# Performance work log

Hardware: AMD Instinct MI355X
Metric: run time of the kernel (lower is better)

Reference implementation:

```python
import jax, jax.numpy as jnp
import numpy as np

EPS = 1e-5

def _layer_norm(x, gamma, beta):
    # LayerNorm over the last two dims [C, 128], matching nn.LayerNorm([C, 128])
    mean = jnp.mean(x, axis=(-2, -1), keepdims=True)
    var = jnp.var(x, axis=(-2, -1), keepdims=True)
    return (x - mean) * jax.lax.rsqrt(var + EPS) * gamma + beta


def setup_inputs() -> dict:
    key = jax.random.key(0)
    ks = jax.random.split(key, 7)
    B, C, N, L = 64, 1024, 128, 512
    W_SCALE = 0.02  # keep pre-softmax logits / activations in a sane range
    return {
        "X_in": jax.random.normal(ks[0], (B, C, N), jnp.float32),
        "T": jax.random.normal(ks[1], (B, C, L), jnp.float32),
        "Wq": jax.random.normal(ks[2], (C, C), jnp.float32) * W_SCALE,
        "Wk": jax.random.normal(ks[3], (C, C), jnp.float32) * W_SCALE,
        "Wv": jax.random.normal(ks[4], (C, C), jnp.float32) * W_SCALE,
        "Wf1": jax.random.normal(ks[5], (C, C), jnp.float32) * W_SCALE,
        "Wf2": jax.random.normal(ks[6], (C, C), jnp.float32) * W_SCALE,
        "gamma": jnp.ones((C, N), jnp.float32),
        "beta": jnp.zeros((C, N), jnp.float32),
    }


def reference(X_in, T, Wq, Wk, Wv, Wf1, Wf2, gamma, beta):
    C = Wq.shape[1]  # feature_map_cs (intended value of the buggy X_in.weight.shape[1])
    # 1x1 Conv1d == per-position channel matmul: weight [out, in]
    q = jnp.einsum('oc,bcn->bon', Wq, X_in)      # [B, C, N]
    k = jnp.einsum('oc,bcl->bol', Wk, T)         # [B, C, L]
    sim = jnp.einsum('bcn,bcl->bnl', q, k) / jnp.sqrt(jnp.float32(C))  # [B, N, L]
    attn = jax.nn.softmax(sim, axis=2)           # softmax over tokens L
    v = jnp.einsum('oc,bcl->bol', Wv, T)         # [B, C, L]
    ctx = jnp.einsum('bcl,bnl->bcn', v, attn)    # [B, C, N] == bmm(values, attn^T)
    X_out = _layer_norm(X_in + ctx, gamma, beta)
    h = jax.nn.relu(jnp.einsum('oc,bcn->bon', Wf1, X_out))
    ffn = jnp.einsum('oc,bcn->bon', Wf2, h)
    return _layer_norm(X_out + ffn, gamma, beta)
```

## Files before the change

### kernel.cpp

```cpp
#include <hip/hip_runtime.h>


using bf16   = __bf16;
using bf16x4 = __attribute__((ext_vector_type(4))) __bf16;
using bf16x8 = __attribute__((ext_vector_type(8))) __bf16;
using f32x4  = __attribute__((ext_vector_type(4))) float;

static constexpr int  Bb = 64;
static constexpr int  Cc = 1024;
static constexpr int  Nn = 128;
static constexpr int  Ll = 512;
static constexpr long long PLANE = (long long)Cc * Nn;
static constexpr float INV_PLANE = 1.0f / 131072.0f;

__device__ __forceinline__ void gload_lds16(const void* g, void* l) {
    __builtin_amdgcn_global_load_lds(
        (__attribute__((address_space(1))) void*)g,
        (__attribute__((address_space(3))) void*)l,
        16, 0, 0);
}

__global__ void __launch_bounds__(256)
prep_all(const float* __restrict__ Wv, const float* __restrict__ Wf1,
         const float* __restrict__ Wf2, const float* __restrict__ Wq,
         const float* __restrict__ Wk, const float* __restrict__ X,
         bf16* __restrict__ WvB, bf16* __restrict__ Wf1B, bf16* __restrict__ Wf2B,
         bf16* __restrict__ WqT, bf16* __restrict__ WkT, bf16* __restrict__ Xt) {
    __shared__ float tile[64][65];
    const int bx = blockIdx.x;
    const int t  = threadIdx.x;
    if (bx < 3072) {
        const float* in = bx < 1024 ? Wv : (bx < 2048 ? Wf1 : Wf2);
        bf16* out       = bx < 1024 ? WvB : (bx < 2048 ? Wf1B : Wf2B);
        int i = (bx & 1023) * 256 + t;
        float4 v = reinterpret_cast<const float4*>(in)[i];
        bf16x4 o = { (bf16)v.x, (bf16)v.y, (bf16)v.z, (bf16)v.w };
        reinterpret_cast<bf16x4*>(out)[i] = o;
        return;
    }
    const float* in; bf16* outT;
    int R, S, bxx, byy, bz = 0;
    if (bx < 3584) {
        int j = bx - 3072;
        in = (j >= 256) ? Wk : Wq; outT = (j >= 256) ? WkT : WqT;
        R = Cc; S = Cc; j &= 255; bxx = j & 15; byy = j >> 4;
    } else {
        int j = bx - 3584; bz = j >> 5; j &= 31;
        bxx = j & 1; byy = j >> 1; in = X; outT = Xt; R = Cc; S = Nn;
    }
    long long plane = (long long)R * S;
    in   += (long long)bz * plane;
    outT += (long long)bz * plane;
    int s0 = bxx * 64, r0 = byy * 64;
    int rl = t >> 4, sc = (t & 15) * 4;
    #pragma unroll
    for (int p = 0; p < 4; ++p) {
        int r = p * 16 + rl;
        float4 v = *(const float4*)(in + (long long)(r0 + r) * S + s0 + sc);
        *(float4*)&tile[r][sc] = v;
    }
    __syncthreads();
    long long tb = ((long long)(s0 >> 6) * (R >> 6) + (r0 >> 6)) * 4096;
    int sb = t >> 3, rg = (t & 7) * 8;
    #pragma unroll
    for (int p = 0; p < 2; ++p) {
        int s = sb + p * 32;
        bf16x8 o;
        #pragma unroll
        for (int j = 0; j < 8; ++j) o[j] = (bf16)tile[rg + j][s];
        *(bf16x8*)(outT + tb + s * 64 + rg) = o;
    }
}

#define GEMM_PROLOGUE_AND_LOOP(A_, Bt_, KLOOP_, LD_, TA_, TB_)                     \
    __shared__ bf16 As[2][128 * 64];                                               \
    __shared__ bf16 Bs[2][128 * 64];                                               \
    const int n0   = blockIdx.x * 128;                                             \
    const int m0   = blockIdx.y * 128;                                             \
    const int t    = threadIdx.x;                                                  \
    const int lane = t & 63;                                                       \
    const int w    = t >> 6;                                                       \
    const int wr   = (w >> 1) * 64;                                                \
    const int wc   = (w & 1) * 64;                                                 \
    const int lr   = lane & 15;                                                    \
    const int hi4  = (lane >> 4) * 16;                                             \
    const int sw   = (lr & 7) << 4;                                                \
    const int stepA_ = (TA_) ? 4096 : 64;                                          \
    const int stepB_ = (TB_) ? 4096 : 64;                                          \
    const bf16* gA[4]; const bf16* gB[4]; int lo[4];                               \
    _Pragma("unroll")                                                              \
    for (int p = 0; p < 4; ++p) {                                                  \
        int o = w * 1024 + lane * 16 + p * 4096;                                   \
        int row = o >> 7;                                                          \
        int scol = ((o & 127) ^ ((row & 7) << 4)) >> 1;                            \
        lo[p] = o;                                                                 \
        int ra = m0 + row, rb = n0 + row;                                          \
        gA[p] = (TA_) ? A_ + ((long long)(ra >> 6) * (LD_ >> 6)) * 4096            \
                           + (ra & 63) * 64 + scol                                 \
                      : A_ + (long long)ra * LD_ + scol;                           \
        gB[p] = (TB_) ? Bt_ + ((long long)(rb >> 6) * (LD_ >> 6)) * 4096           \
                            + (rb & 63) * 64 + scol                                \
                      : Bt_ + (long long)rb * LD_ + scol;                          \
    }                                                                              \
    f32x4 acc[4][4] = {};                                                          \
    const int NT_ = KLOOP_ / 64;                                                   \
    _Pragma("unroll")                                                              \
    for (int p = 0; p < 4; ++p) gload_lds16(gA[p], (char*)As[0] + lo[p]);          \
    _Pragma("unroll")                                                              \
    for (int p = 0; p < 4; ++p) gload_lds16(gB[p], (char*)Bs[0] + lo[p]);          \
    __syncthreads();                                                               \
    int cur_ = 0;                                                                  \
    for (int kt = 0; kt < NT_; ++kt) {                                             \
        if (kt + 1 < NT_) {                                                        \
            _Pragma("unroll")                                                      \
            for (int p = 0; p < 4; ++p)                                            \
                gload_lds16(gA[p] + (long long)(kt + 1) * stepA_,                  \
                            (char*)As[cur_ ^ 1] + lo[p]);                          \
            _Pragma("unroll")                                                      \
            for (int p = 0; p < 4; ++p)                                            \
                gload_lds16(gB[p] + (long long)(kt + 1) * stepB_,                  \
                            (char*)Bs[cur_ ^ 1] + lo[p]);                          \
        }                                                                          \
        const bf16* As_ = As[cur_]; const bf16* Bs_ = Bs[cur_];                    \
        _Pragma("unroll")                                                          \
        for (int kk = 0; kk < 2; ++kk) {                                           \
            bf16x8 af[4], bfr[4];                                                  \
            _Pragma("unroll")                                                      \
            for (int i = 0; i < 4; ++i) {                                          \
                int ra = wr + i * 16 + lr;                                         \
                int rb = wc + i * 16 + lr;                                         \
                af[i]  = *(const bf16x8*)((const char*)As_ +                       \
                          ((((ra << 7) + (kk << 6) + hi4)) ^ sw));                 \
                bfr[i] = *(const bf16x8*)((const char*)Bs_ +                       \
                          ((((rb << 7) + (kk << 6) + hi4)) ^ sw));                 \
            }                                                                      \
            _Pragma("unroll")                                                      \
            for (int mi = 0; mi < 4; ++mi)                                         \
                _Pragma("unroll")                                                  \
                for (int ni = 0; ni < 4; ++ni)                                     \
                    acc[mi][ni] = __builtin_amdgcn_mfma_f32_16x16x32_bf16(         \
                        af[mi], bfr[ni], acc[mi][ni], 0, 0, 0);                    \
        }                                                                          \
        __syncthreads();                                                           \
        cur_ ^= 1;                                                                 \
    }

template <typename OutT, bool RELU, int TA, int TB>
__global__ void __launch_bounds__(256, 2)
gemm_tn(const bf16* __restrict__ A, const bf16* __restrict__ Bt, OutT* __restrict__ C,
        int M, int N, int KLOOP, int ld, long long sA, long long sBt, long long sC,
        float scale) {
    A  += (long long)blockIdx.z * sA;
    Bt += (long long)blockIdx.z * sBt;
    C  += (long long)blockIdx.z * sC;
    GEMM_PROLOGUE_AND_LOOP(A, Bt, KLOOP, ld, TA, TB)
    const int rbase = m0 + wr + (lane >> 4) * 4;
    const int cbase = n0 + wc + lr;
    #pragma unroll
    for (int mi = 0; mi < 4; ++mi)
        #pragma unroll
        for (int ni = 0; ni < 4; ++ni)
            #pragma unroll
            for (int r = 0; r < 4; ++r) {
                float v = acc[mi][ni][r] * scale;
                if (RELU) v = fmaxf(v, 0.0f);
                C[(long long)(rbase + mi * 16 + r) * N + (cbase + ni * 16)] = (OutT)v;
            }
}

__global__ void g2_reduce(const float* __restrict__ p, bf16* __restrict__ g2) {
    int i = (blockIdx.x * 256 + threadIdx.x) * 4;
    float4 a = *(const float4*)(p + i);
    float4 b = *(const float4*)(p + 1048576 + i);
    float4 c = *(const float4*)(p + 2097152 + i);
    float4 d = *(const float4*)(p + 3145728 + i);
    bf16x4 o = { (bf16)(a.x + b.x + c.x + d.x), (bf16)(a.y + b.y + c.y + d.y),
                 (bf16)(a.z + b.z + c.z + d.z), (bf16)(a.w + b.w + c.w + d.w) };
    *(bf16x4*)(g2 + i) = o;
}

__global__ void __launch_bounds__(256, 2)
gemm_sim_exp(const bf16* __restrict__ A , const float* __restrict__ Tg,
             bf16* __restrict__ E, float* __restrict__ rspart) {
    __shared__ char smem[33024];
    bf16* Asb = (bf16*)smem;
    bf16* Bs  = (bf16*)(smem + 16384);
    bf16* scr = (bf16*)(smem + 24576);
    A  += (long long)blockIdx.z * ((long long)Nn * Cc);
    Tg += (long long)blockIdx.z * ((long long)Cc * Ll);
    E  += (long long)blockIdx.z * ((long long)Nn * Ll);
    const int l0 = blockIdx.x * 64;
    const int t = threadIdx.x, lane = t & 63, w = t >> 6;
    const int lr = lane & 15, hi4 = (lane >> 4) * 16, sw = (lr & 7) << 4;
    const bf16* gA[4]; int lo[4];
    #pragma unroll
    for (int p = 0; p < 4; ++p) {
        int o = w * 1024 + lane * 16 + p * 4096;
        int row = o >> 7;
        int scol = ((o & 127) ^ ((row & 7) << 4)) >> 1;
        lo[p] = o;
        gA[p] = A + (long long)row * Cc + scol;
    }
    const int s_c = t >> 2, s_l = (t & 3) * 16;
    float4 treg[4];
    #pragma unroll
    for (int i = 0; i < 4; ++i)
        treg[i] = *(const float4*)(Tg + (long long)s_c * Ll + l0 + s_l + i * 4);
    f32x4 acc[2][4] = {};
    const int NT = Cc / 64;
    for (int kt = 0; kt < NT; ++kt) {
        #pragma unroll
        for (int i = 0; i < 4; ++i) {
            float4 v = treg[i];
            bf16x4 o = { (bf16)v.x, (bf16)v.y, (bf16)v.z, (bf16)v.w };
            *(bf16x4*)(scr + s_c * 66 + s_l + i * 4) = o;
        }
        __syncthreads();
        #pragma unroll
        for (int p = 0; p < 4; ++p) gload_lds16(gA[p] + kt * 64, (char*)Asb + lo[p]);
        {
            int lrow = t & 63;
            #pragma unroll
            for (int p = 0; p < 2; ++p) {
                int c8 = (t >> 6) * 16 + p * 8;
                bf16x8 bv;
                #pragma unroll
                for (int j = 0; j < 8; ++j) bv[j] = scr[(c8 + j) * 66 + lrow];
                *(bf16x8*)((char*)Bs + (((lrow << 7) + c8 * 2) ^ ((lrow & 7) << 4))) = bv;
            }
        }
        if (kt + 1 < NT) {
            #pragma unroll
            for (int i = 0; i < 4; ++i)
                treg[i] = *(const float4*)(Tg + (long long)((kt + 1) * 64 + s_c) * Ll
                                           + l0 + s_l + i * 4);
        }
        __syncthreads();
        #pragma unroll
        for (int kk = 0; kk < 2; ++kk) {
            bf16x8 af[2], bfr[4];
            #pragma unroll
            for (int mi = 0; mi < 2; ++mi) {
                int ra = w * 32 + mi * 16 + lr;
                af[mi] = *(const bf16x8*)((const char*)Asb + (((ra << 7) + (kk << 6) + hi4) ^ sw));
            }
            #pragma unroll
            for (int ni = 0; ni < 4; ++ni) {
                int rb = ni * 16 + lr;
                bfr[ni] = *(const bf16x8*)((const char*)Bs + (((rb << 7) + (kk << 6) + hi4) ^ sw));
            }
            #pragma unroll
            for (int mi = 0; mi < 2; ++mi)
                #pragma unroll
                for (int ni = 0; ni < 4; ++ni)
                    acc[mi][ni] = __builtin_amdgcn_mfma_f32_16x16x32_bf16(
                        af[mi], bfr[ni], acc[mi][ni], 0, 0, 0);
        }
    }
    float psum[2][4];
    #pragma unroll
    for (int mi = 0; mi < 2; ++mi)
        #pragma unroll
        for (int r = 0; r < 4; ++r) psum[mi][r] = 0.f;
    #pragma unroll
    for (int mi = 0; mi < 2; ++mi)
        #pragma unroll
        for (int ni = 0; ni < 4; ++ni)
            #pragma unroll
            for (int r = 0; r < 4; ++r) {
                int row = w * 32 + mi * 16 + (lane >> 4) * 4 + r;
                float ev = __expf(acc[mi][ni][r] * 0.03125f);
                E[(long long)row * Ll + l0 + ni * 16 + lr] = (bf16)ev;
                psum[mi][r] += ev;
            }
    #pragma unroll
    for (int mi = 0; mi < 2; ++mi)
        #pragma unroll
        for (int r = 0; r < 4; ++r) {
            float v = psum[mi][r];
            v += __shfl_xor(v, 1); v += __shfl_xor(v, 2);
            v += __shfl_xor(v, 4); v += __shfl_xor(v, 8);
            psum[mi][r] = v;
        }
    if (lr == 0) {
        float* rp = rspart + ((long long)blockIdx.z * 8 + blockIdx.x) * 128;
        #pragma unroll
        for (int mi = 0; mi < 2; ++mi)
            #pragma unroll
            for (int r = 0; r < 4; ++r)
                rp[w * 32 + mi * 16 + (lane >> 4) * 4 + r] = psum[mi][r];
    }
}

__global__ void __launch_bounds__(256, 4)
gemm_u_scaled(const bf16* __restrict__ A , const float* __restrict__ Tg,
              bf16* __restrict__ C, const float* __restrict__ rspart) {
    __shared__ char smem[40960];
    bf16* AsB = (bf16*)smem;
    bf16* Bs  = (bf16*)(smem + 32768);
    A  += (long long)blockIdx.z * ((long long)Nn * Ll);
    Tg += (long long)blockIdx.z * ((long long)Cc * Ll);
    C  += (long long)blockIdx.z * ((long long)Nn * Cc);
    const float* rp = rspart + (long long)blockIdx.z * 1024;
    const int c0 = blockIdx.x * 64;
    const int t = threadIdx.x, lane = t & 63, w = t >> 6;
    const int lr = lane & 15, hi4 = (lane >> 4) * 16, sw = (lr & 7) << 4;
    const bf16* gA[4]; int lo[4];
    #pragma unroll
    for (int p = 0; p < 4; ++p) {
        int o = w * 1024 + lane * 16 + p * 4096;
        int row = o >> 7;
        int scol = ((o & 127) ^ ((row & 7) << 4)) >> 1;
        lo[p] = o;
        gA[p] = A + (long long)row * Ll + scol;
    }
    const int s_c = t >> 2, s_l = (t & 3) * 16;
    float4 treg[4];
    #pragma unroll
    for (int p = 0; p < 4; ++p) gload_lds16(gA[p], (char*)AsB + lo[p]);
    #pragma unroll
    for (int i = 0; i < 4; ++i)
        treg[i] = *(const float4*)(Tg + (long long)(c0 + s_c) * Ll + s_l + i * 4);
    f32x4 acc[2][4] = {};
    int cur = 0;
    const int NT = Ll / 64;
    for (int kt = 0; kt < NT; ++kt) {
        if (kt + 1 < NT) {
            #pragma unroll
            for (int p = 0; p < 4; ++p)
                gload_lds16(gA[p] + (kt + 1) * 64, (char*)AsB + (cur ^ 1) * 16384 + lo[p]);
        }
        __syncthreads();
        #pragma unroll
        for (int p = 0; p < 2; ++p) {
            bf16x8 bv;
            #pragma unroll
            for (int j = 0; j < 4; ++j) {
                bv[j]     = (bf16)((const float*)&treg[p * 2])[j];
                bv[4 + j] = (bf16)((const float*)&treg[p * 2 + 1])[j];
            }
            *(bf16x8*)((char*)Bs + (((s_c << 7) + (s_l + p * 8) * 2) ^ ((s_c & 7) << 4))) = bv;
        }
        if (kt + 1 < NT) {
            #pragma unroll
            for (int i = 0; i < 4; ++i)
                treg[i] = *(const float4*)(Tg + (long long)(c0 + s_c) * Ll
                                           + (kt + 1) * 64 + s_l + i * 4);
        }
        __syncthreads();
        const bf16* As_ = AsB + cur * 8192;
        #pragma unroll
        for (int kk = 0; kk < 2; ++kk) {
            bf16x8 af[2], bfr[4];
            #pragma unroll
            for (int mi = 0; mi < 2; ++mi) {
                int ra = w * 32 + mi * 16 + lr;
                af[mi] = *(const bf16x8*)((const char*)As_ + (((ra << 7) + (kk << 6) + hi4) ^ sw));
            }
            #pragma unroll
            for (int ni = 0; ni < 4; ++ni) {
                int rb = ni * 16 + lr;
                bfr[ni] = *(const bf16x8*)((const char*)Bs + (((rb << 7) + (kk << 6) + hi4) ^ sw));
            }
            #pragma unroll
            for (int mi = 0; mi < 2; ++mi)
                #pragma unroll
                for (int ni = 0; ni < 4; ++ni)
                    acc[mi][ni] = __builtin_amdgcn_mfma_f32_16x16x32_bf16(
                        af[mi], bfr[ni], acc[mi][ni], 0, 0, 0);
        }
        cur ^= 1;
    }
    #pragma unroll
    for (int mi = 0; mi < 2; ++mi)
        #pragma unroll
        for (int r = 0; r < 4; ++r) {
            int row = w * 32 + mi * 16 + (lane >> 4) * 4 + r;
            float s = 0.f;
            #pragma unroll
            for (int j = 0; j < 8; ++j) s += rp[j * 128 + row];
            float inv = 1.f / s;
            #pragma unroll
            for (int ni = 0; ni < 4; ++ni)
                C[(long long)row * Cc + (c0 + ni * 16 + lr)] = (bf16)(acc[mi][ni][r] * inv);
        }
}

__global__ void __launch_bounds__(256, 2)
gemm_ctx_ln1(const bf16* __restrict__ A , const bf16* __restrict__ Bt ,
             const float* __restrict__ X, bf16* __restrict__ Z1, float* __restrict__ partials,
             int K, long long sBt) {
    const int N = Nn;
    Bt += (long long)blockIdx.z * sBt;
    X  += (long long)blockIdx.z * PLANE;
    Z1 += (long long)blockIdx.z * PLANE;
    GEMM_PROLOGUE_AND_LOOP(A, Bt, K, K, 0, 0)
    const int rbase = m0 + wr + (lane >> 4) * 4;
    const int cbase = n0 + wc + lr;
    float s = 0.f, ss = 0.f;
    #pragma unroll
    for (int mi = 0; mi < 4; ++mi)
        #pragma unroll
        for (int ni = 0; ni < 4; ++ni)
            #pragma unroll
            for (int r = 0; r < 4; ++r) {
                long long idx = (long long)(rbase + mi * 16 + r) * N + (cbase + ni * 16);
                float zv = acc[mi][ni][r] + X[idx];
                Z1[idx] = (bf16)zv;
                s += zv; ss += zv * zv;
            }
    #pragma unroll
    for (int off = 32; off; off >>= 1) { s += __shfl_xor(s, off); ss += __shfl_xor(ss, off); }
    __shared__ float red[8];
    if (lane == 0) { red[w] = s; red[4 + w] = ss; }
    __syncthreads();
    if (t == 0) {
        float S = red[0] + red[1] + red[2] + red[3];
        float SS = red[4] + red[5] + red[6] + red[7];
        float* p = partials + ((long long)blockIdx.z * 8 + blockIdx.y) * 2;
        p[0] = S; p[1] = SS;
    }
}

__global__ void __launch_bounds__(256, 2)
gemm_ffn_ln2(const bf16* __restrict__ A , const bf16* __restrict__ Bt ,
             const bf16* __restrict__ Z1, const float* __restrict__ pp1,
             const float* __restrict__ gamma, const float* __restrict__ beta,
             bf16* __restrict__ Z2, float* __restrict__ partials,
             int K, long long sA) {
    A  += (long long)blockIdx.z * sA;
    Z1 += (long long)blockIdx.z * PLANE;
    Z2 += (long long)blockIdx.z * PLANE;
    float S1 = 0.f, SS1 = 0.f;
    #pragma unroll
    for (int j = 0; j < 8; ++j) {
        S1  += pp1[((long long)blockIdx.z * 8 + j) * 2];
        SS1 += pp1[((long long)blockIdx.z * 8 + j) * 2 + 1];
    }
    const float mean1 = S1 * INV_PLANE;
    const float rstd1 = rsqrtf(SS1 * INV_PLANE - mean1 * mean1 + 1e-5f);
    GEMM_PROLOGUE_AND_LOOP(A, Bt, K, K, 0, 0)
    const int rbase = m0 + wr + (lane >> 4) * 4;
    const int cbase = n0 + wc + lr;
    float s = 0.f, ss = 0.f;
    #pragma unroll
    for (int mi = 0; mi < 4; ++mi)
        #pragma unroll
        for (int ni = 0; ni < 4; ++ni) {
            long long a = (long long)(cbase + ni * 16) * Nn + rbase + mi * 16;
            bf16x4 z1v = *(const bf16x4*)(Z1 + a);
            float4 g  = *(const float4*)(gamma + a);
            float4 be = *(const float4*)(beta + a);
            float x0 = ((float)z1v[0] - mean1) * rstd1 * g.x + be.x;
            float x1 = ((float)z1v[1] - mean1) * rstd1 * g.y + be.y;
            float x2 = ((float)z1v[2] - mean1) * rstd1 * g.z + be.z;
            float x3 = ((float)z1v[3] - mean1) * rstd1 * g.w + be.w;
            float z0 = acc[mi][ni][0] + x0, z1 = acc[mi][ni][1] + x1;
            float z2 = acc[mi][ni][2] + x2, z3 = acc[mi][ni][3] + x3;
            bf16x4 zo = { (bf16)z0, (bf16)z1, (bf16)z2, (bf16)z3 };
            *(bf16x4*)(Z2 + a) = zo;
            s  += z0 + z1 + z2 + z3;
            ss += z0 * z0 + z1 * z1 + z2 * z2 + z3 * z3;
        }
    #pragma unroll
    for (int off = 32; off; off >>= 1) { s += __shfl_xor(s, off); ss += __shfl_xor(ss, off); }
    __shared__ float red[8];
    if (lane == 0) { red[w] = s; red[4 + w] = ss; }
    __syncthreads();
    if (t == 0) {
        float S = red[0] + red[1] + red[2] + red[3];
        float SS = red[4] + red[5] + red[6] + red[7];
        float* p = partials + ((long long)blockIdx.z * 8 + blockIdx.x) * 2;
        p[0] = S; p[1] = SS;
    }
}

__global__ void ln1_norm_transpose(const bf16* __restrict__ Z1, const float* __restrict__ partials,
                                   const float* __restrict__ gamma, const float* __restrict__ beta,
                                   bf16* __restrict__ XoutT) {
    int b = blockIdx.z;
    float S = 0.f, SS = 0.f;
    #pragma unroll
    for (int j = 0; j < 8; ++j) {
        S  += partials[((long long)b * 8 + j) * 2];
        SS += partials[((long long)b * 8 + j) * 2 + 1];
    }
    float mean = S * INV_PLANE;
    float rstd = rsqrtf(SS * INV_PLANE - mean * mean + 1e-5f);
    __shared__ float tile[64][65];
    long long base = (long long)b * PLANE;
    int n0 = blockIdx.x * 64, c0 = blockIdx.y * 64;
    int t = threadIdx.x;
    int rl = t >> 4, sc = (t & 15) * 4;
    #pragma unroll
    for (int p = 0; p < 4; ++p) {
        int r = p * 16 + rl;
        long long idx = (long long)(c0 + r) * Nn + n0 + sc;
        bf16x4 z  = *(const bf16x4*)(Z1 + base + idx);
        float4 g  = *(const float4*)(gamma + idx);
        float4 be = *(const float4*)(beta + idx);
        float4 o = {((float)z[0] - mean) * rstd * g.x + be.x,
                    ((float)z[1] - mean) * rstd * g.y + be.y,
                    ((float)z[2] - mean) * rstd * g.z + be.z,
                    ((float)z[3] - mean) * rstd * g.w + be.w};
        *(float4*)&tile[r][sc] = o;
    }
    __syncthreads();
    long long tb = ((long long)(n0 >> 6) * (Cc >> 6) + (c0 >> 6)) * 4096;
    int sb = t >> 3, rg = (t & 7) * 8;
    #pragma unroll
    for (int p = 0; p < 2; ++p) {
        int n = sb + p * 32;
        bf16x8 o;
        #pragma unroll
        for (int j = 0; j < 8; ++j) o[j] = (bf16)tile[rg + j][n];
        *(bf16x8*)(XoutT + base + tb + n * 64 + rg) = o;
    }
}

__global__ void ln2_final(const bf16* __restrict__ Z2, const float* __restrict__ partials,
                          const float* __restrict__ gamma, const float* __restrict__ beta,
                          float* __restrict__ out) {
    int b = blockIdx.y;
    float S = 0.f, SS = 0.f;
    #pragma unroll
    for (int j = 0; j < 8; ++j) {
        S  += partials[((long long)b * 8 + j) * 2];
        SS += partials[((long long)b * 8 + j) * 2 + 1];
    }
    float mean = S * INV_PLANE;
    float rstd = rsqrtf(SS * INV_PLANE - mean * mean + 1e-5f);
    long long base = (long long)b * PLANE;
    int i = (blockIdx.x * 256 + threadIdx.x) * 8;
    bf16x8 z = *(const bf16x8*)(Z2 + base + i);
    #pragma unroll
    for (int h = 0; h < 2; ++h) {
        float4 g  = *(const float4*)(gamma + i + h * 4);
        float4 be = *(const float4*)(beta + i + h * 4);
        float4 o = {((float)z[h * 4 + 0] - mean) * rstd * g.x + be.x,
                    ((float)z[h * 4 + 1] - mean) * rstd * g.y + be.y,
                    ((float)z[h * 4 + 2] - mean) * rstd * g.z + be.z,
                    ((float)z[h * 4 + 3] - mean) * rstd * g.w + be.w};
        *(float4*)(out + base + i + h * 4) = o;
    }
}

extern "C" void kernel_launch(void* const* d_in, const int* in_sizes, int n_in,
                              void* d_out, int out_size, void* d_ws, size_t ws_size,
                              hipStream_t stream) {
    const float* X   = (const float*)d_in[0];
    const float* T   = (const float*)d_in[1];
    const float* Wq  = (const float*)d_in[2];
    const float* Wk  = (const float*)d_in[3];
    const float* Wv  = (const float*)d_in[4];
    const float* Wf1 = (const float*)d_in[5];
    const float* Wf2 = (const float*)d_in[6];
    const float* gamma = (const float*)d_in[7];
    const float* beta  = (const float*)d_in[8];
    float* out = (float*)d_out;
    char* ws = (char*)d_ws;
    const size_t MB = 1ull << 20;

    bf16* WvB  = (bf16*)(ws + 0 * MB);
    bf16* Wf1B = (bf16*)(ws + 2 * MB);
    bf16* Wf2B = (bf16*)(ws + 4 * MB);
    bf16* WqT  = (bf16*)(ws + 6 * MB);
    bf16* WkT  = (bf16*)(ws + 8 * MB);
    bf16* G2   = (bf16*)(ws + 10 * MB);
    bf16* Xt   = (bf16*)(ws + 12 * MB);
    bf16* Z1   = (bf16*)(ws + 28 * MB);
    bf16* XoutT= (bf16*)(ws + 44 * MB);
    bf16* hT   = (bf16*)(ws + 60 * MB);
    bf16* e    = (bf16*)(ws + 76 * MB);
    bf16* Z2   = (bf16*)(ws + 92 * MB);
    bf16* E    = (bf16*)(ws + 108 * MB);
    bf16* u    = (bf16*)(ws + 116 * MB);
    float* G2p = (float*)(ws + 132 * MB);
    float* pp1 = (float*)(ws + 148 * MB);
    float* pp2 = (float*)(ws + 148 * MB + 65536);
    float* rsp = (float*)(ws + 149 * MB);

    dim3 blk256(256);

    prep_all<<<dim3(5632), blk256, 0, stream>>>(
        Wv, Wf1, Wf2, Wq, Wk, X, WvB, Wf1B, Wf2B, WqT, WkT, Xt);

    gemm_tn<float, false, 1, 1><<<dim3(8, 8, 4), blk256, 0, stream>>>(
        WkT, WqT, G2p, Cc, Cc, 256, Cc, 16384, 16384, 1048576, 1.f);
    g2_reduce<<<dim3(1024), blk256, 0, stream>>>(G2p, G2);

    gemm_tn<bf16, false, 1, 0><<<dim3(8, 1, Bb), blk256, 0, stream>>>(
        Xt, G2, e, Nn, Cc, Cc, Cc, (long long)Nn * Cc, 0, (long long)Nn * Cc, 1.f);
    gemm_sim_exp<<<dim3(8, 1, Bb), blk256, 0, stream>>>(e, T, E, rsp);
    gemm_u_scaled<<<dim3(16, 1, Bb), blk256, 0, stream>>>(E, T, u, rsp);
    gemm_ctx_ln1<<<dim3(1, 8, Bb), blk256, 0, stream>>>(
        WvB, u, X, Z1, pp1, Cc, (long long)Nn * Cc);
    ln1_norm_transpose<<<dim3(Nn / 64, Cc / 64, Bb), blk256, 0, stream>>>(
        Z1, pp1, gamma, beta, XoutT);
    gemm_tn<bf16, true, 1, 0><<<dim3(8, 1, Bb), blk256, 0, stream>>>(
        XoutT, Wf1B, hT, Nn, Cc, Cc, Cc, (long long)Nn * Cc, 0, (long long)Nn * Cc, 1.f);
    gemm_ffn_ln2<<<dim3(8, 1, Bb), blk256, 0, stream>>>(
        hT, Wf2B, Z1, pp1, gamma, beta, Z2, pp2, Cc, (long long)Nn * Cc);
    ln2_final<<<dim3(64, Bb), blk256, 0, stream>>>(Z2, pp2, gamma, beta, out);
}
```

Baseline: 258.0 us.

## Fuse fp32-to-bf16 conversion of weights and X into GEMM operand loads

Drops the upfront conversion and transpose of Wv, Wf1, Wf2 and X to bf16. Four GEMM kernels now load fp32 operands straight from global memory into registers, convert them to bf16 and write them swizzled into LDS. For X this includes an in-LDS transpose through a scratch buffer, with the next tile prefetched into registers. This removes a prep pass and its global round-trip. In exchange, every batch block re-reads and re-converts the fp32 weights, doubling operand bytes and adding conversion ALU work inside the main loops, which are now single-buffered for that operand.

```diff
diff --git a/kernel.cpp b/kernel.cpp
--- a/kernel.cpp
+++ b/kernel.cpp
@@ -21,53 +21,32 @@
 }
 
 __global__ void __launch_bounds__(256)
-prep_all(const float* __restrict__ Wv, const float* __restrict__ Wf1,
-         const float* __restrict__ Wf2, const float* __restrict__ Wq,
-         const float* __restrict__ Wk, const float* __restrict__ X,
-         bf16* __restrict__ WvB, bf16* __restrict__ Wf1B, bf16* __restrict__ Wf2B,
-         bf16* __restrict__ WqT, bf16* __restrict__ WkT, bf16* __restrict__ Xt) {
+prep_w(const float* __restrict__ Wq, const float* __restrict__ Wk,
+       bf16* __restrict__ WqT, bf16* __restrict__ WkT) {
     __shared__ float tile[64][65];
-    const int bx = blockIdx.x;
-    const int t  = threadIdx.x;
-    if (bx < 3072) {
-        const float* in = bx < 1024 ? Wv : (bx < 2048 ? Wf1 : Wf2);
-        bf16* out       = bx < 1024 ? WvB : (bx < 2048 ? Wf1B : Wf2B);
-        int i = (bx & 1023) * 256 + t;
-        float4 v = reinterpret_cast<const float4*>(in)[i];
-        bf16x4 o = { (bf16)v.x, (bf16)v.y, (bf16)v.z, (bf16)v.w };
-        reinterpret_cast<bf16x4*>(out)[i] = o;
-        return;
-    }
-    const float* in; bf16* outT;
-    int R, S, bxx, byy, bz = 0;
-    if (bx < 3584) {
-        int j = bx - 3072;
-        in = (j >= 256) ? Wk : Wq; outT = (j >= 256) ? WkT : WqT;
-        R = Cc; S = Cc; j &= 255; bxx = j & 15; byy = j >> 4;
-    } else {
-        int j = bx - 3584; bz = j >> 5; j &= 31;
-        bxx = j & 1; byy = j >> 1; in = X; outT = Xt; R = Cc; S = Nn;
-    }
-    long long plane = (long long)R * S;
-    in   += (long long)bz * plane;
-    outT += (long long)bz * plane;
+    int j = blockIdx.x;
+    const float* in = (j >= 256) ? Wk : Wq;
+    bf16* outT      = (j >= 256) ? WkT : WqT;
+    j &= 255;
+    int bxx = j & 15, byy = j >> 4;
     int s0 = bxx * 64, r0 = byy * 64;
+    int t = threadIdx.x;
     int rl = t >> 4, sc = (t & 15) * 4;
     #pragma unroll
     for (int p = 0; p < 4; ++p) {
         int r = p * 16 + rl;
-        float4 v = *(const float4*)(in + (long long)(r0 + r) * S + s0 + sc);
+        float4 v = *(const float4*)(in + (long long)(r0 + r) * Cc + s0 + sc);
         *(float4*)&tile[r][sc] = v;
     }
     __syncthreads();
-    long long tb = ((long long)(s0 >> 6) * (R >> 6) + (r0 >> 6)) * 4096;
+    long long tb = ((long long)(s0 >> 6) * (Cc >> 6) + (r0 >> 6)) * 4096;
     int sb = t >> 3, rg = (t & 7) * 8;
     #pragma unroll
     for (int p = 0; p < 2; ++p) {
         int s = sb + p * 32;
         bf16x8 o;
         #pragma unroll
-        for (int j = 0; j < 8; ++j) o[j] = (bf16)tile[rg + j][s];
+        for (int jj = 0; jj < 8; ++jj) o[jj] = (bf16)tile[rg + jj][s];
         *(bf16x8*)(outT + tb + s * 64 + rg) = o;
     }
 }
@@ -180,6 +159,92 @@
 }
 
 __global__ void __launch_bounds__(256, 2)
+gemm_e(const float* __restrict__ Xg, const bf16* __restrict__ G2, bf16* __restrict__ e) {
+    __shared__ char smem[49664];
+    bf16* Asl = (bf16*)smem;
+    bf16* Bs  = (bf16*)(smem + 16384);
+    bf16* scr = (bf16*)(smem + 32768);
+    Xg += (long long)blockIdx.z * PLANE;
+    e  += (long long)blockIdx.z * ((long long)Nn * Cc);
+    const int n0 = blockIdx.x * 128;
+    const int t = threadIdx.x, lane = t & 63, w = t >> 6;
+    const int wr = (w >> 1) * 64, wc = (w & 1) * 64;
+    const int lr = lane & 15, hi4 = (lane >> 4) * 16, sw = (lr & 7) << 4;
+    const bf16* gB[4]; int lo[4];
+    #pragma unroll
+    for (int p = 0; p < 4; ++p) {
+        int o = w * 1024 + lane * 16 + p * 4096;
+        int row = o >> 7;
+        int scol = ((o & 127) ^ ((row & 7) << 4)) >> 1;
+        lo[p] = o;
+        gB[p] = G2 + (long long)(n0 + row) * Cc + scol;
+    }
+    const int s_c = t >> 2, s_n = (t & 3) * 32;
+    float4 xreg[8];
+    #pragma unroll
+    for (int i = 0; i < 8; ++i)
+        xreg[i] = *(const float4*)(Xg + (long long)s_c * Nn + s_n + i * 4);
+    f32x4 acc[4][4] = {};
+    const int NT = Cc / 64;
+    for (int kt = 0; kt < NT; ++kt) {
+        #pragma unroll
+        for (int i = 0; i < 8; ++i) {
+            float4 v = xreg[i];
+            bf16x4 o = { (bf16)v.x, (bf16)v.y, (bf16)v.z, (bf16)v.w };
+            *(bf16x4*)(scr + s_c * 130 + s_n + i * 4) = o;
+        }
+        __syncthreads();
+        #pragma unroll
+        for (int p = 0; p < 4; ++p) gload_lds16(gB[p] + kt * 64, (char*)Bs + lo[p]);
+        {
+            int nrow = t & 127;
+            #pragma unroll
+            for (int g = 0; g < 4; ++g) {
+                int c0 = (t >> 7) * 32 + g * 8;
+                bf16x8 bv;
+                #pragma unroll
+                for (int j = 0; j < 8; ++j) bv[j] = scr[(c0 + j) * 130 + nrow];
+                *(bf16x8*)((char*)Asl + (((nrow << 7) + c0 * 2) ^ ((nrow & 7) << 4))) = bv;
+            }
+        }
+        if (kt + 1 < NT) {
+            #pragma unroll
+            for (int i = 0; i < 8; ++i)
+                xreg[i] = *(const float4*)(Xg + (long long)((kt + 1) * 64 + s_c) * Nn
+                                           + s_n + i * 4);
+        }
+        __syncthreads();
+        #pragma unroll
+        for (int kk = 0; kk < 2; ++kk) {
+            bf16x8 af[4], bfr[4];
+            #pragma unroll
+            for (int i = 0; i < 4; ++i) {
+                int ra = wr + i * 16 + lr;
+                int rb = wc + i * 16 + lr;
+                af[i]  = *(const bf16x8*)((const char*)Asl + (((ra << 7) + (kk << 6) + hi4) ^ sw));
+                bfr[i] = *(const bf16x8*)((const char*)Bs  + (((rb << 7) + (kk << 6) + hi4) ^ sw));
+            }
+            #pragma unroll
+            for (int mi = 0; mi < 4; ++mi)
+                #pragma unroll
+                for (int ni = 0; ni < 4; ++ni)
+                    acc[mi][ni] = __builtin_amdgcn_mfma_f32_16x16x32_bf16(
+                        af[mi], bfr[ni], acc[mi][ni], 0, 0, 0);
+        }
+    }
+    const int rbase = wr + (lane >> 4) * 4;
+    const int cbase = n0 + wc + lr;
+    #pragma unroll
+    for (int mi = 0; mi < 4; ++mi)
+        #pragma unroll
+        for (int ni = 0; ni < 4; ++ni)
+            #pragma unroll
+            for (int r = 0; r < 4; ++r)
+                e[(long long)(rbase + mi * 16 + r) * Cc + (cbase + ni * 16)] =
+                    (bf16)acc[mi][ni][r];
+}
+
+__global__ void __launch_bounds__(256, 2)
 gemm_sim_exp(const bf16* __restrict__ A , const float* __restrict__ Tg,
              bf16* __restrict__ E, float* __restrict__ rspart) {
     __shared__ char smem[33024];
@@ -387,16 +452,76 @@
 }
 
 __global__ void __launch_bounds__(256, 2)
-gemm_ctx_ln1(const bf16* __restrict__ A , const bf16* __restrict__ Bt ,
-             const float* __restrict__ X, bf16* __restrict__ Z1, float* __restrict__ partials,
-             int K, long long sBt) {
-    const int N = Nn;
-    Bt += (long long)blockIdx.z * sBt;
+gemm_ctx_ln1(const float* __restrict__ Wv, const bf16* __restrict__ U,
+             const float* __restrict__ X, bf16* __restrict__ Z1, float* __restrict__ partials) {
+    __shared__ char smem[32768];
+    bf16* Asl = (bf16*)smem;
+    bf16* Bs  = (bf16*)(smem + 16384);
+    U  += (long long)blockIdx.z * ((long long)Nn * Cc);
     X  += (long long)blockIdx.z * PLANE;
     Z1 += (long long)blockIdx.z * PLANE;
-    GEMM_PROLOGUE_AND_LOOP(A, Bt, K, K, 0, 0)
+    const int m0 = blockIdx.y * 128;
+    const int t = threadIdx.x, lane = t & 63, w = t >> 6;
+    const int wr = (w >> 1) * 64, wc = (w & 1) * 64;
+    const int lr = lane & 15, hi4 = (lane >> 4) * 16, sw = (lr & 7) << 4;
+    const bf16* gB[4]; int lo[4];
+    #pragma unroll
+    for (int p = 0; p < 4; ++p) {
+        int o = w * 1024 + lane * 16 + p * 4096;
+        int row = o >> 7;
+        int scol = ((o & 127) ^ ((row & 7) << 4)) >> 1;
+        lo[p] = o;
+        gB[p] = U + (long long)row * Cc + scol;
+    }
+    const int s_r = t >> 1, s_k = (t & 1) * 32;
+    float4 wreg[8];
+    #pragma unroll
+    for (int i = 0; i < 8; ++i)
+        wreg[i] = *(const float4*)(Wv + (long long)(m0 + s_r) * Cc + s_k + i * 4);
+    f32x4 acc[4][4] = {};
+    const int NT = Cc / 64;
+    for (int kt = 0; kt < NT; ++kt) {
+        __syncthreads();
+        #pragma unroll
+        for (int p = 0; p < 4; ++p) gload_lds16(gB[p] + kt * 64, (char*)Bs + lo[p]);
+        #pragma unroll
+        for (int p = 0; p < 4; ++p) {
+            int kc = s_k + p * 8;
+            bf16x8 bv;
+            #pragma unroll
+            for (int j = 0; j < 4; ++j) {
+                bv[j]     = (bf16)((const float*)&wreg[p * 2])[j];
+                bv[4 + j] = (bf16)((const float*)&wreg[p * 2 + 1])[j];
+            }
+            *(bf16x8*)((char*)Asl + (((s_r << 7) + kc * 2) ^ ((s_r & 7) << 4))) = bv;
+        }
+        if (kt + 1 < NT) {
+            #pragma unroll
+            for (int i = 0; i < 8; ++i)
+                wreg[i] = *(const float4*)(Wv + (long long)(m0 + s_r) * Cc
+                                           + (kt + 1) * 64 + s_k + i * 4);
+        }
+        __syncthreads();
+        #pragma unroll
+        for (int kk = 0; kk < 2; ++kk) {
+            bf16x8 af[4], bfr[4];
+            #pragma unroll
+            for (int i = 0; i < 4; ++i) {
+                int ra = wr + i * 16 + lr;
+                int rb = wc + i * 16 + lr;
+                af[i]  = *(const bf16x8*)((const char*)Asl + (((ra << 7) + (kk << 6) + hi4) ^ sw));
+                bfr[i] = *(const bf16x8*)((const char*)Bs  + (((rb << 7) + (kk << 6) + hi4) ^ sw));
+            }
+            #pragma unroll
+            for (int mi = 0; mi < 4; ++mi)
+                #pragma unroll
+                for (int ni = 0; ni < 4; ++ni)
+                    acc[mi][ni] = __builtin_amdgcn_mfma_f32_16x16x32_bf16(
+                        af[mi], bfr[ni], acc[mi][ni], 0, 0, 0);
+        }
+    }
     const int rbase = m0 + wr + (lane >> 4) * 4;
-    const int cbase = n0 + wc + lr;
+    const int cbase = wc + lr;
     float s = 0.f, ss = 0.f;
     #pragma unroll
     for (int mi = 0; mi < 4; ++mi)
@@ -404,7 +529,7 @@
         for (int ni = 0; ni < 4; ++ni)
             #pragma unroll
             for (int r = 0; r < 4; ++r) {
-                long long idx = (long long)(rbase + mi * 16 + r) * N + (cbase + ni * 16);
+                long long idx = (long long)(rbase + mi * 16 + r) * Nn + (cbase + ni * 16);
                 float zv = acc[mi][ni][r] + X[idx];
                 Z1[idx] = (bf16)zv;
                 s += zv; ss += zv * zv;
@@ -423,12 +548,94 @@
 }
 
 __global__ void __launch_bounds__(256, 2)
-gemm_ffn_ln2(const bf16* __restrict__ A , const bf16* __restrict__ Bt ,
+gemm_h(const bf16* __restrict__ XoutT, const float* __restrict__ Wf1, bf16* __restrict__ hT) {
+    __shared__ char smem[32768];
+    bf16* Asl = (bf16*)smem;
+    bf16* Bs  = (bf16*)(smem + 16384);
+    XoutT += (long long)blockIdx.z * PLANE;
+    hT    += (long long)blockIdx.z * ((long long)Nn * Cc);
+    const int n0 = blockIdx.x * 128;
+    const int t = threadIdx.x, lane = t & 63, w = t >> 6;
+    const int wr = (w >> 1) * 64, wc = (w & 1) * 64;
+    const int lr = lane & 15, hi4 = (lane >> 4) * 16, sw = (lr & 7) << 4;
+    const bf16* gA[4]; int lo[4];
+    #pragma unroll
+    for (int p = 0; p < 4; ++p) {
+        int o = w * 1024 + lane * 16 + p * 4096;
+        int row = o >> 7;
+        int scol = ((o & 127) ^ ((row & 7) << 4)) >> 1;
+        lo[p] = o;
+        gA[p] = XoutT + ((long long)(row >> 6) * (Cc >> 6)) * 4096 + (row & 63) * 64 + scol;
+    }
+    const int s_r = t >> 1, s_k = (t & 1) * 32;
+    float4 wreg[8];
+    #pragma unroll
+    for (int i = 0; i < 8; ++i)
+        wreg[i] = *(const float4*)(Wf1 + (long long)(n0 + s_r) * Cc + s_k + i * 4);
+    f32x4 acc[4][4] = {};
+    const int NT = Cc / 64;
+    for (int kt = 0; kt < NT; ++kt) {
+        __syncthreads();
+        #pragma unroll
+        for (int p = 0; p < 4; ++p)
+            gload_lds16(gA[p] + (long long)kt * 4096, (char*)Asl + lo[p]);
+        #pragma unroll
+        for (int p = 0; p < 4; ++p) {
+            int kc = s_k + p * 8;
+            bf16x8 bv;
+            #pragma unroll
+            for (int j = 0; j < 4; ++j) {
+                bv[j]     = (bf16)((const float*)&wreg[p * 2])[j];
+                bv[4 + j] = (bf16)((const float*)&wreg[p * 2 + 1])[j];
+            }
+            *(bf16x8*)((char*)Bs + (((s_r << 7) + kc * 2) ^ ((s_r & 7) << 4))) = bv;
+        }
+        if (kt + 1 < NT) {
+            #pragma unroll
+            for (int i = 0; i < 8; ++i)
+                wreg[i] = *(const float4*)(Wf1 + (long long)(n0 + s_r) * Cc
+                                           + (kt + 1) * 64 + s_k + i * 4);
+        }
+        __syncthreads();
+        #pragma unroll
+        for (int kk = 0; kk < 2; ++kk) {
+            bf16x8 af[4], bfr[4];
+            #pragma unroll
+            for (int i = 0; i < 4; ++i) {
+                int ra = wr + i * 16 + lr;
+                int rb = wc + i * 16 + lr;
+                af[i]  = *(const bf16x8*)((const char*)Asl + (((ra << 7) + (kk << 6) + hi4) ^ sw));
+                bfr[i] = *(const bf16x8*)((const char*)Bs  + (((rb << 7) + (kk << 6) + hi4) ^ sw));
+            }
+            #pragma unroll
+            for (int mi = 0; mi < 4; ++mi)
+                #pragma unroll
+                for (int ni = 0; ni < 4; ++ni)
+                    acc[mi][ni] = __builtin_amdgcn_mfma_f32_16x16x32_bf16(
+                        af[mi], bfr[ni], acc[mi][ni], 0, 0, 0);
+        }
+    }
+    const int rbase = wr + (lane >> 4) * 4;
+    const int cbase = n0 + wc + lr;
+    #pragma unroll
+    for (int mi = 0; mi < 4; ++mi)
+        #pragma unroll
+        for (int ni = 0; ni < 4; ++ni)
+            #pragma unroll
+            for (int r = 0; r < 4; ++r)
+                hT[(long long)(rbase + mi * 16 + r) * Cc + (cbase + ni * 16)] =
+                    (bf16)fmaxf(acc[mi][ni][r], 0.0f);
+}
+
+__global__ void __launch_bounds__(256, 2)
+gemm_ffn_ln2(const bf16* __restrict__ HT, const float* __restrict__ Wf2,
              const bf16* __restrict__ Z1, const float* __restrict__ pp1,
              const float* __restrict__ gamma, const float* __restrict__ beta,
-             bf16* __restrict__ Z2, float* __restrict__ partials,
-             int K, long long sA) {
-    A  += (long long)blockIdx.z * sA;
+             bf16* __restrict__ Z2, float* __restrict__ partials) {
+    __shared__ char smem[32768];
+    bf16* Asl = (bf16*)smem;
+    bf16* Bs  = (bf16*)(smem + 16384);
+    HT += (long long)blockIdx.z * ((long long)Nn * Cc);
     Z1 += (long long)blockIdx.z * PLANE;
     Z2 += (long long)blockIdx.z * PLANE;
     float S1 = 0.f, SS1 = 0.f;
@@ -439,8 +646,67 @@
     }
     const float mean1 = S1 * INV_PLANE;
     const float rstd1 = rsqrtf(SS1 * INV_PLANE - mean1 * mean1 + 1e-5f);
-    GEMM_PROLOGUE_AND_LOOP(A, Bt, K, K, 0, 0)
-    const int rbase = m0 + wr + (lane >> 4) * 4;
+    const int n0 = blockIdx.x * 128;
+    const int t = threadIdx.x, lane = t & 63, w = t >> 6;
+    const int wr = (w >> 1) * 64, wc = (w & 1) * 64;
+    const int lr = lane & 15, hi4 = (lane >> 4) * 16, sw = (lr & 7) << 4;
+    const bf16* gA[4]; int lo[4];
+    #pragma unroll
+    for (int p = 0; p < 4; ++p) {
+        int o = w * 1024 + lane * 16 + p * 4096;
+        int row = o >> 7;
+        int scol = ((o & 127) ^ ((row & 7) << 4)) >> 1;
+        lo[p] = o;
+        gA[p] = HT + (long long)row * Cc + scol;
+    }
+    const int s_r = t >> 1, s_k = (t & 1) * 32;
+    float4 wreg[8];
+    #pragma unroll
+    for (int i = 0; i < 8; ++i)
+        wreg[i] = *(const float4*)(Wf2 + (long long)(n0 + s_r) * Cc + s_k + i * 4);
+    f32x4 acc[4][4] = {};
+    const int NT = Cc / 64;
+    for (int kt = 0; kt < NT; ++kt) {
+        __syncthreads();
+        #pragma unroll
+        for (int p = 0; p < 4; ++p) gload_lds16(gA[p] + kt * 64, (char*)Asl + lo[p]);
+        #pragma unroll
+        for (int p = 0; p < 4; ++p) {
+            int kc = s_k + p * 8;
+            bf16x8 bv;
+            #pragma unroll
+            for (int j = 0; j < 4; ++j) {
+                bv[j]     = (bf16)((const float*)&wreg[p * 2])[j];
+                bv[4 + j] = (bf16)((const float*)&wreg[p * 2 + 1])[j];
+            }
+            *(bf16x8*)((char*)Bs + (((s_r << 7) + kc * 2) ^ ((s_r & 7) << 4))) = bv;
+        }
+        if (kt + 1 < NT) {
+            #pragma unroll
+            for (int i = 0; i < 8; ++i)
+                wreg[i] = *(const float4*)(Wf2 + (long long)(n0 + s_r) * Cc
+                                           + (kt + 1) * 64 + s_k + i * 4);
+        }
+        __syncthreads();
+        #pragma unroll
+        for (int kk = 0; kk < 2; ++kk) {
+            bf16x8 af[4], bfr[4];
+            #pragma unroll
+            for (int i = 0; i < 4; ++i) {
+                int ra = wr + i * 16 + lr;
+                int rb = wc + i * 16 + lr;
+                af[i]  = *(const bf16x8*)((const char*)Asl + (((ra << 7) + (kk << 6) + hi4) ^ sw));
+                bfr[i] = *(const bf16x8*)((const char*)Bs  + (((rb << 7) + (kk << 6) + hi4) ^ sw));
+            }
+            #pragma unroll
+            for (int mi = 0; mi < 4; ++mi)
+                #pragma unroll
+                for (int ni = 0; ni < 4; ++ni)
+                    acc[mi][ni] = __builtin_amdgcn_mfma_f32_16x16x32_bf16(
+                        af[mi], bfr[ni], acc[mi][ni], 0, 0, 0);
+        }
+    }
+    const int rbase = wr + (lane >> 4) * 4;
     const int cbase = n0 + wc + lr;
     float s = 0.f, ss = 0.f;
     #pragma unroll
@@ -561,45 +827,35 @@
     char* ws = (char*)d_ws;
     const size_t MB = 1ull << 20;
 
-    bf16* WvB  = (bf16*)(ws + 0 * MB);
-    bf16* Wf1B = (bf16*)(ws + 2 * MB);
-    bf16* Wf2B = (bf16*)(ws + 4 * MB);
-    bf16* WqT  = (bf16*)(ws + 6 * MB);
-    bf16* WkT  = (bf16*)(ws + 8 * MB);
-    bf16* G2   = (bf16*)(ws + 10 * MB);
-    bf16* Xt   = (bf16*)(ws + 12 * MB);
-    bf16* Z1   = (bf16*)(ws + 28 * MB);
-    bf16* XoutT= (bf16*)(ws + 44 * MB);
-    bf16* hT   = (bf16*)(ws + 60 * MB);
-    bf16* e    = (bf16*)(ws + 76 * MB);
-    bf16* Z2   = (bf16*)(ws + 92 * MB);
-    bf16* E    = (bf16*)(ws + 108 * MB);
-    bf16* u    = (bf16*)(ws + 116 * MB);
-    float* G2p = (float*)(ws + 132 * MB);
-    float* pp1 = (float*)(ws + 148 * MB);
-    float* pp2 = (float*)(ws + 148 * MB + 65536);
-    float* rsp = (float*)(ws + 149 * MB);
+    bf16* WqT  = (bf16*)(ws + 0 * MB);
+    bf16* WkT  = (bf16*)(ws + 2 * MB);
+    bf16* G2   = (bf16*)(ws + 4 * MB);
+    float* G2p = (float*)(ws + 6 * MB);
+    bf16* e    = (bf16*)(ws + 22 * MB);
+    bf16* E    = (bf16*)(ws + 38 * MB);
+    bf16* u    = (bf16*)(ws + 46 * MB);
+    bf16* Z1   = (bf16*)(ws + 62 * MB);
+    bf16* XoutT= (bf16*)(ws + 78 * MB);
+    bf16* hT   = (bf16*)(ws + 94 * MB);
+    bf16* Z2   = (bf16*)(ws + 110 * MB);
+    float* pp1 = (float*)(ws + 126 * MB);
+    float* pp2 = (float*)(ws + 126 * MB + 65536);
+    float* rsp = (float*)(ws + 127 * MB);
 
     dim3 blk256(256);
 
-    prep_all<<<dim3(5632), blk256, 0, stream>>>(
-        Wv, Wf1, Wf2, Wq, Wk, X, WvB, Wf1B, Wf2B, WqT, WkT, Xt);
-
+    prep_w<<<dim3(512), blk256, 0, stream>>>(Wq, Wk, WqT, WkT);
     gemm_tn<float, false, 1, 1><<<dim3(8, 8, 4), blk256, 0, stream>>>(
         WkT, WqT, G2p, Cc, Cc, 256, Cc, 16384, 16384, 1048576, 1.f);
     g2_reduce<<<dim3(1024), blk256, 0, stream>>>(G2p, G2);
-
-    gemm_tn<bf16, false, 1, 0><<<dim3(8, 1, Bb), blk256, 0, stream>>>(
-        Xt, G2, e, Nn, Cc, Cc, Cc, (long long)Nn * Cc, 0, (long long)Nn * Cc, 1.f);
+    gemm_e<<<dim3(8, 1, Bb), blk256, 0, stream>>>(X, G2, e);
     gemm_sim_exp<<<dim3(8, 1, Bb), blk256, 0, stream>>>(e, T, E, rsp);
     gemm_u_scaled<<<dim3(16, 1, Bb), blk256, 0, stream>>>(E, T, u, rsp);
-    gemm_ctx_ln1<<<dim3(1, 8, Bb), blk256, 0, stream>>>(
-        WvB, u, X, Z1, pp1, Cc, (long long)Nn * Cc);
+    gemm_ctx_ln1<<<dim3(1, 8, Bb), blk256, 0, stream>>>(Wv, u, X, Z1, pp1);
     ln1_norm_transpose<<<dim3(Nn / 64, Cc / 64, Bb), blk256, 0, stream>>>(
         Z1, pp1, gamma, beta, XoutT);
-    gemm_tn<bf16, true, 1, 0><<<dim3(8, 1, Bb), blk256, 0, stream>>>(
-        XoutT, Wf1B, hT, Nn, Cc, Cc, Cc, (long long)Nn * Cc, 0, (long long)Nn * Cc, 1.f);
+    gemm_h<<<dim3(8, 1, Bb), blk256, 0, stream>>>(XoutT, Wf1, hT);
     gemm_ffn_ln2<<<dim3(8, 1, Bb), blk256, 0, stream>>>(
-        hT, Wf2B, Z1, pp1, gamma, beta, Z2, pp2, Cc, (long long)Nn * Cc);
+        hT, Wf2, Z1, pp1, gamma, beta, Z2, pp2);
     ln2_final<<<dim3(64, Bb), blk256, 0, stream>>>(Z2, pp2, gamma, beta, out);
 }
```

Result: slower. 340.8 us (+32.1%).
